# Performance work log

Hardware: AMD Instinct MI355X
Metric: run time of the kernel (lower is better)

## Reference

```python
import jax, jax.numpy as jnp
import numpy as np

B, S, DIN, DOUT = 4, 2048, 4096, 16384

def setup_inputs() -> dict:
    key = jax.random.key(0)
    k1, k2, k3 = jax.random.split(key, 3)
    x = jax.random.normal(k1, (B, S, DIN), dtype=jnp.float32)
    # int8 palettized weights in [-127, 127] (palette_size=255 -> signed 127)
    weight_i8 = jax.random.randint(k2, (DOUT, DIN), -127, 128, dtype=jnp.int8)
    # scalar symmetric scaling factor (max_abs / 127 in the original)
    scale = jnp.float32(0.01)
    bias = jax.random.normal(k3, (DOUT,), dtype=jnp.float32)
    return {"x": x, "weight_i8": weight_i8, "scale": scale, "bias": bias}

def reference(x, weight_i8, scale, bias):
    # Dequantize: int8 -> fp32 * scalar scale, then F.linear(x, W, b) = x @ W.T + b
    full_w = weight_i8.astype(jnp.float32) * scale  # [DOUT, DIN]
    return jnp.einsum('bsi,oi->bso', x, full_w) + bias
```

## Files before the change

### kernel.cpp

```cpp
#include <hip/hip_runtime.h>
#include <hip/hip_bf16.h>

typedef __attribute__((ext_vector_type(4))) float f32x4;
typedef __attribute__((ext_vector_type(4))) int   i32x4;
typedef __attribute__((ext_vector_type(8))) short s16x8;
typedef unsigned short ushort_t;

#define MDIM 8192
#define KDIM 4096
#define NDIM 16384
#define NKT  64

static __device__ __forceinline__ short f2bf(float f) {
    __bf16 h = (__bf16)f;
    return __builtin_bit_cast(short, h);
}

static __device__ __forceinline__ void gload_lds16(const void* g, void* l) {
    __builtin_amdgcn_global_load_lds(
        (const __attribute__((address_space(1))) unsigned int*)g,
        (__attribute__((address_space(3))) unsigned int*)l,
        16, 0, 0);
}


__global__ __launch_bounds__(256)
void prep_all(const float* __restrict__ X, const int* __restrict__ W,
              char* __restrict__ Xq, char* __restrict__ Wq8,
              float* __restrict__ sx)
{
    const int b = blockIdx.x;
    const int t = threadIdx.x;
    if (b < MDIM) {
        __shared__ float wmax[4];
        const float* xr = X + (size_t)b * KDIM;
        f32x4 v[4];
        #pragma unroll
        for (int p = 0; p < 4; ++p) v[p] = ((const f32x4*)xr)[t * 4 + p];
        float m = 0.f;
        #pragma unroll
        for (int p = 0; p < 4; ++p)
            #pragma unroll
            for (int q = 0; q < 4; ++q)
                m = fmaxf(m, fabsf(v[p][q]));
        #pragma unroll
        for (int off = 32; off >= 1; off >>= 1)
            m = fmaxf(m, __shfl_xor(m, off));
        if ((t & 63) == 0) wmax[t >> 6] = m;
        __syncthreads();
        m = fmaxf(fmaxf(wmax[0], wmax[1]), fmaxf(wmax[2], wmax[3]));
        const float inv = 127.0f / fmaxf(m, 1e-30f);
        if (t == 0) sx[b] = m * (1.0f / 127.0f);
        int pk[4];
        #pragma unroll
        for (int p = 0; p < 4; ++p) {
            int q0 = min(127, max(-127, __float2int_rn(v[p][0] * inv)));
            int q1 = min(127, max(-127, __float2int_rn(v[p][1] * inv)));
            int q2 = min(127, max(-127, __float2int_rn(v[p][2] * inv)));
            int q3 = min(127, max(-127, __float2int_rn(v[p][3] * inv)));
            pk[p] = (q0 & 255) | ((q1 & 255) << 8) | ((q2 & 255) << 16) | ((q3 & 255) << 24);
        }
        ((i32x4*)(Xq + (size_t)b * KDIM))[t] = *(i32x4*)pk;
    } else {
        const int n16 = NDIM * (KDIM / 16);
        for (int idx = (b - MDIM) * 256 + t; idx < n16; idx += 2048 * 256) {
            int pk[4];
            #pragma unroll
            for (int p = 0; p < 4; ++p) {
                i32x4 a = ((const i32x4*)W)[idx * 4 + p];
                pk[p] = (a[0] & 255) | ((a[1] & 255) << 8) |
                        ((a[2] & 255) << 16) | ((a[3] & 255) << 24);
            }
            ((i32x4*)Wq8)[idx] = *(i32x4*)pk;
        }
    }
}


#define BAR()   __builtin_amdgcn_s_barrier()
#define SB0()   __builtin_amdgcn_sched_barrier(0)
#define PRIO(N) __builtin_amdgcn_s_setprio(N)
#define LGKM4() do { asm volatile("s_waitcnt lgkmcnt(4)" ::: "memory"); SB0(); } while (0)
#define LGKM8() do { asm volatile("s_waitcnt lgkmcnt(8)" ::: "memory"); SB0(); } while (0)
#define VM6()   asm volatile("s_waitcnt vmcnt(6)" ::: "memory")

#define MM16(M0, PA, PB)                                                       \
    PRIO(1);                                                                   \
    _Pragma("unroll")                                                          \
    for (int mi = 0; mi < 4; ++mi)                                             \
      _Pragma("unroll")                                                        \
      for (int nn = 0; nn < 4; ++nn)                                           \
        acc[(M0) + mi][nn] = __builtin_amdgcn_mfma_i32_16x16x64_i8(            \
            PA[mi], PB[nn], acc[(M0) + mi][nn], 0, 0, 0);                      \
    PRIO(0);

#define ITER4(RB0, RB1, RB2, WB0, WB1, T)                                      \
  {                                                                            \
    const char* r0 = ldsc + (RB0);                                             \
    const char* r1 = ldsc + (RB1);                                             \
    const char* r2 = ldsc + (RB2);                                             \
    char* w0 = ldsc + (WB0);                                                   \
    char* w1 = ldsc + (WB1);                                                   \
    const size_t ko3 = (size_t)(((T) + 3) & (NKT - 1)) * 64;                   \
    const size_t ko4 = (size_t)(((T) + 4) & (NKT - 1)) * 64;                   \
          \
    PAo[0] = *(const i32x4*)(r0 + aoff[4]);                                    \
    PAo[1] = *(const i32x4*)(r0 + aoff[5]);                                    \
    PAo[2] = *(const i32x4*)(r0 + aoff[6]);                                    \
    PAo[3] = *(const i32x4*)(r0 + aoff[7]);                                    \
    gload_lds16(pA0 + ko3, w0 + 0 + ldsw);                                     \
    gload_lds16(pA1 + ko3, w0 + 8192 + ldsw);                                  \
    BAR(); LGKM4(); MM16(0, PAe, BF); VM6(); BAR();                            \
        \
    BG[0]  = *(const i32x4*)(r1 + boff[0]);                                    \
    BG[1]  = *(const i32x4*)(r1 + boff[1]);                                    \
    BG[2]  = *(const i32x4*)(r1 + boff[2]);                                    \
    BG[3]  = *(const i32x4*)(r1 + boff[3]);                                    \
    PAe[0] = *(const i32x4*)(r1 + aoff[0]);                                    \
    PAe[1] = *(const i32x4*)(r1 + aoff[1]);                                    \
    PAe[2] = *(const i32x4*)(r1 + aoff[2]);                                    \
    PAe[3] = *(const i32x4*)(r1 + aoff[3]);                                    \
    gload_lds16(pB0 + ko3, w0 + 16384 + ldsw);                                 \
    gload_lds16(pB1 + ko3, w0 + 24576 + ldsw);                                 \
    BAR(); LGKM8(); MM16(4, PAo, BF); BAR();                                   \
                \
    PAo[0] = *(const i32x4*)(r1 + aoff[4]);                                    \
    PAo[1] = *(const i32x4*)(r1 + aoff[5]);                                    \
    PAo[2] = *(const i32x4*)(r1 + aoff[6]);                                    \
    PAo[3] = *(const i32x4*)(r1 + aoff[7]);                                    \
    gload_lds16(pA0 + ko4, w1 + 0 + ldsw);                                     \
    gload_lds16(pA1 + ko4, w1 + 8192 + ldsw);                                  \
    BAR(); LGKM4(); MM16(0, PAe, BG); VM6(); BAR();                            \
        \
    BF[0]  = *(const i32x4*)(r2 + boff[0]);                                    \
    BF[1]  = *(const i32x4*)(r2 + boff[1]);                                    \
    BF[2]  = *(const i32x4*)(r2 + boff[2]);                                    \
    BF[3]  = *(const i32x4*)(r2 + boff[3]);                                    \
    PAe[0] = *(const i32x4*)(r2 + aoff[0]);                                    \
    PAe[1] = *(const i32x4*)(r2 + aoff[1]);                                    \
    PAe[2] = *(const i32x4*)(r2 + aoff[2]);                                    \
    PAe[3] = *(const i32x4*)(r2 + aoff[3]);                                    \
    gload_lds16(pB0 + ko4, w1 + 16384 + ldsw);                                 \
    gload_lds16(pB1 + ko4, w1 + 24576 + ldsw);                                 \
    BAR(); LGKM8(); MM16(4, PAo, BG); BAR();                                   \
  }

__global__ __launch_bounds__(512, 2)
void sl_gemm_i8q(const char* __restrict__ A, const char* __restrict__ Bw,
                 const float* __restrict__ sx,
                 const float* __restrict__ scale_p, const float* __restrict__ bias,
                 float* __restrict__ Out)
{
    __shared__ char ldsbuf[131072];
    char* ldsc = ldsbuf;

    const int t    = threadIdx.x;
    const int lane = t & 63;
    const int wave = t >> 6;
    const int wr   = wave >> 2;
    const int wc   = wave & 3;

    int bid = blockIdx.x;
    int tm = ((bid & 7) << 2) + ((bid >> 3) & 3);
    int tn = bid >> 5;
    const int m0 = tm << 8;
    const int n0 = tn << 8;

    const int srow  = wave * 16 + (lane >> 2);
    const int sslot = lane & 3;
    const int sA    = sslot ^ ((srow >> 1) & 3);
    const char* pA0 = A  + (size_t)(m0 + srow) * KDIM + sA * 16;
    const char* pA1 = pA0 + (size_t)128 * KDIM;
    const char* pB0 = Bw + (size_t)(n0 + srow) * KDIM + sA * 16;
    const char* pB1 = pB0 + (size_t)128 * KDIM;
    const int ldsw = wave * 1024;

    const int fr = lane & 15;
    const int fs = lane >> 4;
    int aoff[8], boff[4];
    #pragma unroll
    for (int i = 0; i < 8; ++i) {
        int ra = wr * 128 + i * 16 + fr;
        aoff[i] = ra * 64 + ((fs ^ ((ra >> 1) & 3)) * 16);
    }
    #pragma unroll
    for (int j = 0; j < 4; ++j) {
        int rb = wc * 64 + j * 16 + fr;
        boff[j] = 16384 + rb * 64 + ((fs ^ ((rb >> 1) & 3)) * 16);
    }

    i32x4 acc[8][4];
    #pragma unroll
    for (int i = 0; i < 8; ++i)
        #pragma unroll
        for (int j = 0; j < 4; ++j)
            acc[i][j] = (i32x4){0, 0, 0, 0};

    i32x4 PAe[4], PAo[4], BF[4], BG[4];

    #pragma unroll
    for (int kt = 0; kt < 3; ++kt) {
        const size_t ko = (size_t)kt * 64;
        char* b = ldsc + kt * 32768;
        gload_lds16(pA0 + ko, b + ldsw);
        gload_lds16(pA1 + ko, b + 8192  + ldsw);
        gload_lds16(pB0 + ko, b + 16384 + ldsw);
        gload_lds16(pB1 + ko, b + 24576 + ldsw);
    }
    asm volatile("s_waitcnt vmcnt(8)" ::: "memory");
    BAR();
    SB0();

    BF[0]  = *(const i32x4*)(ldsc + boff[0]);
    BF[1]  = *(const i32x4*)(ldsc + boff[1]);
    BF[2]  = *(const i32x4*)(ldsc + boff[2]);
    BF[3]  = *(const i32x4*)(ldsc + boff[3]);
    PAe[0] = *(const i32x4*)(ldsc + aoff[0]);
    PAe[1] = *(const i32x4*)(ldsc + aoff[1]);
    PAe[2] = *(const i32x4*)(ldsc + aoff[2]);
    PAe[3] = *(const i32x4*)(ldsc + aoff[3]);

    for (int tt = 0; tt < NKT; tt += 4) {
        ITER4(0 * 32768, 1 * 32768, 2 * 32768, 3 * 32768, 0 * 32768, tt);
        ITER4(2 * 32768, 3 * 32768, 0 * 32768, 1 * 32768, 2 * 32768, tt + 2);
    }

    const float scale = scale_p[0];
    #pragma unroll
    for (int i = 0; i < 8; ++i) {
        const int r0 = m0 + wr * 128 + i * 16 + fs * 4;
        float s4[4];
        #pragma unroll
        for (int q = 0; q < 4; ++q) s4[q] = sx[r0 + q] * scale;
        #pragma unroll
        for (int j = 0; j < 4; ++j) {
            const int c   = n0 + wc * 64 + j * 16 + fr;
            const float bj = bias[c];
            float* op = Out + (size_t)r0 * NDIM + c;
            #pragma unroll
            for (int q = 0; q < 4; ++q)
                op[(size_t)q * NDIM] = (float)acc[i][j][q] * s4[q] + bj;
        }
    }
}


__global__ __launch_bounds__(256, 2)
void sl_gemm_fb(const float* __restrict__ X, const int* __restrict__ Wq,
                const float* __restrict__ scale_p, const float* __restrict__ bias,
                float* __restrict__ Out)
{
    __shared__ s16x8 As[128 * 4];
    __shared__ s16x8 Bs[128 * 4];

    const int t    = threadIdx.x;
    const int lane = t & 63;
    const int wave = t >> 6;
    const int wr   = wave >> 1;
    const int wc   = wave & 1;

    int bid = blockIdx.x;
    int swz = (bid & 7) * 1024 + (bid >> 3);
    int panel   = swz >> 10;
    int inpanel = swz & 1023;
    int tn = (panel << 4) + (inpanel >> 6);
    int tm = inpanel & 63;
    const int m0 = tm << 7;
    const int n0 = tn << 7;

    const int srow  = t >> 1;
    const int shalf = t & 1;
    const float* Xp = X  + (size_t)(m0 + srow) * KDIM + shalf * 16;
    const int*   Wp = Wq + (size_t)(n0 + srow) * KDIM + shalf * 16;

    f32x4 acc[4][4];
    #pragma unroll
    for (int i = 0; i < 4; ++i)
        #pragma unroll
        for (int j = 0; j < 4; ++j)
            acc[i][j] = (f32x4){0.f, 0.f, 0.f, 0.f};

    const int fr = lane & 15;
    const int fs = lane >> 4;

    f32x4 ar[4];
    i32x4 br[4];
    #pragma unroll
    for (int p = 0; p < 4; ++p) {
        ar[p] = *(const f32x4*)(Xp + p * 4);
        br[p] = *(const i32x4*)(Wp + p * 4);
    }

    const int wbase = srow * 4;
    const int wswz  = (srow >> 1) & 3;
    const int ws0   = (shalf * 2)     ^ wswz;
    const int ws1   = (shalf * 2 + 1) ^ wswz;

    for (int kt = 0; kt < KDIM / 32; ++kt) {
        __syncthreads();
        {
            s16x8 v0, v1;
            #pragma unroll
            for (int q = 0; q < 8; ++q) v0[q] = f2bf(ar[q >> 2][q & 3]);
            #pragma unroll
            for (int q = 0; q < 8; ++q) v1[q] = f2bf(ar[2 + (q >> 2)][q & 3]);
            As[wbase + ws0] = v0;
            As[wbase + ws1] = v1;
            s16x8 u0, u1;
            #pragma unroll
            for (int q = 0; q < 8; ++q) u0[q] = f2bf((float)br[q >> 2][q & 3]);
            #pragma unroll
            for (int q = 0; q < 8; ++q) u1[q] = f2bf((float)br[2 + (q >> 2)][q & 3]);
            Bs[wbase + ws0] = u0;
            Bs[wbase + ws1] = u1;
        }
        __syncthreads();

        if (kt + 1 < KDIM / 32) {
            const float* Xn = Xp + (size_t)(kt + 1) * 32;
            const int*   Wn = Wp + (size_t)(kt + 1) * 32;
            #pragma unroll
            for (int p = 0; p < 4; ++p) {
                ar[p] = *(const f32x4*)(Xn + p * 4);
                br[p] = *(const i32x4*)(Wn + p * 4);
            }
        }

        s16x8 af[4], bq[4];
        #pragma unroll
        for (int i = 0; i < 4; ++i) {
            int row = wr * 64 + i * 16 + fr;
            af[i] = As[row * 4 + (fs ^ ((row >> 1) & 3))];
        }
        #pragma unroll
        for (int j = 0; j < 4; ++j) {
            int col = wc * 64 + j * 16 + fr;
            bq[j] = Bs[col * 4 + (fs ^ ((col >> 1) & 3))];
        }
        #pragma unroll
        for (int i = 0; i < 4; ++i)
            #pragma unroll
            for (int j = 0; j < 4; ++j)
                acc[i][j] = __builtin_amdgcn_mfma_f32_16x16x32_bf16(
                    af[i], bq[j], acc[i][j], 0, 0, 0);
    }

    const float scale = scale_p[0];
    #pragma unroll
    for (int j = 0; j < 4; ++j) {
        const int c  = n0 + wc * 64 + j * 16 + fr;
        const float bj = bias[c];
        #pragma unroll
        for (int i = 0; i < 4; ++i) {
            const int r0 = m0 + wr * 64 + i * 16 + fs * 4;
            float* op = Out + (size_t)r0 * NDIM + c;
            #pragma unroll
            for (int q = 0; q < 4; ++q)
                op[(size_t)q * NDIM] = acc[i][j][q] * scale + bj;
        }
    }
}

extern "C" void kernel_launch(void* const* d_in, const int* in_sizes, int n_in,
                              void* d_out, int out_size, void* d_ws, size_t ws_size,
                              hipStream_t stream) {
    const float* X     = (const float*)d_in[0];
    const int*   Wq    = (const int*)d_in[1];
    const float* scale = (const float*)d_in[2];
    const float* bias  = (const float*)d_in[3];
    float*       Out   = (float*)d_out;

    const size_t xqB = (size_t)MDIM * KDIM;
    const size_t wqB = (size_t)NDIM * KDIM;
    const size_t sxB = (size_t)MDIM * sizeof(float);
    if (ws_size >= xqB + wqB + sxB) {
        char*  Xq  = (char*)d_ws;
        char*  Wq8 = (char*)d_ws + xqB;
        float* sx  = (float*)((char*)d_ws + xqB + wqB);
        hipLaunchKernelGGL(prep_all, dim3(MDIM + 2048), dim3(256), 0, stream,
                           X, Wq, Xq, Wq8, sx);
        hipLaunchKernelGGL(sl_gemm_i8q, dim3(2048), dim3(512), 0, stream,
                           Xq, Wq8, sx, scale, bias, Out);
    } else {
        hipLaunchKernelGGL(sl_gemm_fb, dim3(8192), dim3(256), 0, stream,
                           X, Wq, scale, bias, Out);
    }
}
```

Before: 660.5 us.

## Deepen int8 GEMM prefetch to four stages and halve barriers per k-tile

Reworks the main loop of the int8 MFMA GEMM so that a full k-tile (A and B halves) is staged into LDS in one batch, after the buffer has been fully consumed. The prologue preloads four tiles instead of three. The per-tile schedule drops from four barriers to one, with a vmcnt(4) wait. This cuts synchronisation stalls and lets global-to-LDS loads run further ahead of the MFMA work. In exchange the loads are issued in larger bursts and there are fewer interleaving points, which changes how well memory latency hides behind compute.

```diff
diff --git a/kernel.cpp b/kernel.cpp
--- a/kernel.cpp
+++ b/kernel.cpp
@@ -82,7 +82,7 @@
 #define PRIO(N) __builtin_amdgcn_s_setprio(N)
 #define LGKM4() do { asm volatile("s_waitcnt lgkmcnt(4)" ::: "memory"); SB0(); } while (0)
 #define LGKM8() do { asm volatile("s_waitcnt lgkmcnt(8)" ::: "memory"); SB0(); } while (0)
-#define VM6()   asm volatile("s_waitcnt vmcnt(6)" ::: "memory")
+#define VM4()   asm volatile("s_waitcnt vmcnt(4)" ::: "memory")
 
 #define MM16(M0, PA, PB)                                                       \
     PRIO(1);                                                                   \
@@ -94,24 +94,26 @@
             PA[mi], PB[nn], acc[(M0) + mi][nn], 0, 0, 0);                      \
     PRIO(0);
 
-#define ITER4(RB0, RB1, RB2, WB0, WB1, T)                                      \
+#define STG4(KO, WB)                                                           \
+    gload_lds16(pA0 + (KO), ldsc + (WB) + 0     + ldsw);                       \
+    gload_lds16(pA1 + (KO), ldsc + (WB) + 8192  + ldsw);                       \
+    gload_lds16(pB0 + (KO), ldsc + (WB) + 16384 + ldsw);                       \
+    gload_lds16(pB1 + (KO), ldsc + (WB) + 24576 + ldsw);
+
+#define ITER2(RB0, RB1, RB2, T)                                                \
   {                                                                            \
     const char* r0 = ldsc + (RB0);                                             \
     const char* r1 = ldsc + (RB1);                                             \
     const char* r2 = ldsc + (RB2);                                             \
-    char* w0 = ldsc + (WB0);                                                   \
-    char* w1 = ldsc + (WB1);                                                   \
-    const size_t ko3 = (size_t)(((T) + 3) & (NKT - 1)) * 64;                   \
     const size_t ko4 = (size_t)(((T) + 4) & (NKT - 1)) * 64;                   \
-          \
+    const size_t ko5 = (size_t)(((T) + 5) & (NKT - 1)) * 64;                   \
+                                            \
     PAo[0] = *(const i32x4*)(r0 + aoff[4]);                                    \
     PAo[1] = *(const i32x4*)(r0 + aoff[5]);                                    \
     PAo[2] = *(const i32x4*)(r0 + aoff[6]);                                    \
     PAo[3] = *(const i32x4*)(r0 + aoff[7]);                                    \
-    gload_lds16(pA0 + ko3, w0 + 0 + ldsw);                                     \
-    gload_lds16(pA1 + ko3, w0 + 8192 + ldsw);                                  \
-    BAR(); LGKM4(); MM16(0, PAe, BF); VM6(); BAR();                            \
-        \
+    LGKM4();                                                                   \
+    MM16(0, PAe, BF);                                                          \
     BG[0]  = *(const i32x4*)(r1 + boff[0]);                                    \
     BG[1]  = *(const i32x4*)(r1 + boff[1]);                                    \
     BG[2]  = *(const i32x4*)(r1 + boff[2]);                                    \
@@ -120,18 +122,19 @@
     PAe[1] = *(const i32x4*)(r1 + aoff[1]);                                    \
     PAe[2] = *(const i32x4*)(r1 + aoff[2]);                                    \
     PAe[3] = *(const i32x4*)(r1 + aoff[3]);                                    \
-    gload_lds16(pB0 + ko3, w0 + 16384 + ldsw);                                 \
-    gload_lds16(pB1 + ko3, w0 + 24576 + ldsw);                                 \
-    BAR(); LGKM8(); MM16(4, PAo, BF); BAR();                                   \
-                \
+    LGKM8();                                                                   \
+    MM16(4, PAo, BF);                                                          \
+    VM4();                                                                     \
+    BAR();                                                                     \
+    SB0();                                                                     \
+    STG4(ko4, RB0);                                                            \
+                                          \
     PAo[0] = *(const i32x4*)(r1 + aoff[4]);                                    \
     PAo[1] = *(const i32x4*)(r1 + aoff[5]);                                    \
     PAo[2] = *(const i32x4*)(r1 + aoff[6]);                                    \
     PAo[3] = *(const i32x4*)(r1 + aoff[7]);                                    \
-    gload_lds16(pA0 + ko4, w1 + 0 + ldsw);                                     \
-    gload_lds16(pA1 + ko4, w1 + 8192 + ldsw);                                  \
-    BAR(); LGKM4(); MM16(0, PAe, BG); VM6(); BAR();                            \
-        \
+    LGKM4();                                                                   \
+    MM16(0, PAe, BG);                                                          \
     BF[0]  = *(const i32x4*)(r2 + boff[0]);                                    \
     BF[1]  = *(const i32x4*)(r2 + boff[1]);                                    \
     BF[2]  = *(const i32x4*)(r2 + boff[2]);                                    \
@@ -140,16 +143,19 @@
     PAe[1] = *(const i32x4*)(r2 + aoff[1]);                                    \
     PAe[2] = *(const i32x4*)(r2 + aoff[2]);                                    \
     PAe[3] = *(const i32x4*)(r2 + aoff[3]);                                    \
-    gload_lds16(pB0 + ko4, w1 + 16384 + ldsw);                                 \
-    gload_lds16(pB1 + ko4, w1 + 24576 + ldsw);                                 \
-    BAR(); LGKM8(); MM16(4, PAo, BG); BAR();                                   \
+    LGKM8();                                                                   \
+    MM16(4, PAo, BG);                                                          \
+    VM4();                                                                     \
+    BAR();                                                                     \
+    SB0();                                                                     \
+    STG4(ko5, RB1);                                                            \
   }
 
 __global__ __launch_bounds__(512, 2)
-void sl_gemm_i8q(const char* __restrict__ A, const char* __restrict__ Bw,
-                 const float* __restrict__ sx,
-                 const float* __restrict__ scale_p, const float* __restrict__ bias,
-                 float* __restrict__ Out)
+void sl_gemm_i8s2(const char* __restrict__ A, const char* __restrict__ Bw,
+                  const float* __restrict__ sx,
+                  const float* __restrict__ scale_p, const float* __restrict__ bias,
+                  float* __restrict__ Out)
 {
     __shared__ char ldsbuf[131072];
     char* ldsc = ldsbuf;
@@ -199,13 +205,9 @@
     i32x4 PAe[4], PAo[4], BF[4], BG[4];
 
     #pragma unroll
-    for (int kt = 0; kt < 3; ++kt) {
+    for (int kt = 0; kt < 4; ++kt) {
         const size_t ko = (size_t)kt * 64;
-        char* b = ldsc + kt * 32768;
-        gload_lds16(pA0 + ko, b + ldsw);
-        gload_lds16(pA1 + ko, b + 8192  + ldsw);
-        gload_lds16(pB0 + ko, b + 16384 + ldsw);
-        gload_lds16(pB1 + ko, b + 24576 + ldsw);
+        STG4(ko, kt * 32768);
     }
     asm volatile("s_waitcnt vmcnt(8)" ::: "memory");
     BAR();
@@ -221,8 +223,8 @@
     PAe[3] = *(const i32x4*)(ldsc + aoff[3]);
 
     for (int tt = 0; tt < NKT; tt += 4) {
-        ITER4(0 * 32768, 1 * 32768, 2 * 32768, 3 * 32768, 0 * 32768, tt);
-        ITER4(2 * 32768, 3 * 32768, 0 * 32768, 1 * 32768, 2 * 32768, tt + 2);
+        ITER2(0 * 32768, 1 * 32768, 2 * 32768, tt);
+        ITER2(2 * 32768, 3 * 32768, 0 * 32768, tt + 2);
     }
 
     const float scale = scale_p[0];
@@ -379,7 +381,7 @@
         float* sx  = (float*)((char*)d_ws + xqB + wqB);
         hipLaunchKernelGGL(prep_all, dim3(MDIM + 2048), dim3(256), 0, stream,
                            X, Wq, Xq, Wq8, sx);
-        hipLaunchKernelGGL(sl_gemm_i8q, dim3(2048), dim3(512), 0, stream,
+        hipLaunchKernelGGL(sl_gemm_i8s2, dim3(2048), dim3(512), 0, stream,
                            Xq, Wq8, sx, scale, bias, Out);
     } else {
         hipLaunchKernelGGL(sl_gemm_fb, dim3(8192), dim3(256), 0, stream,
```

Result: no change. 665.4 us (+0.8%).
